# Performance work log

Measured on AMD Instinct MI355X. Metric: run time of the kernel, lower is better.

Reference implementation:

```python
import jax, jax.numpy as jnp
import numpy as np

B, N, K, D, M, KEY_DIM = 2, 16384, 32, 128, 2, 64


def _mlp(x, w_in, b_in, w_hid, b_hid, w_out, b_out, act):
    # FCBlock: in->hidden, 3 hidden layers, hidden->out; activation on all but last.
    h = act(x @ w_in + b_in)
    for i in range(w_hid.shape[0]):
        h = act(h @ w_hid[i] + b_hid[i])
    return h @ w_out + b_out


def setup_inputs() -> dict:
    key = jax.random.key(0)
    ks = jax.random.split(key, 16)
    rn = lambda k, s, sc=1.0: jax.random.normal(k, s, dtype=jnp.float32) * sc
    w_scale = 0.05  # small init so sigmoid/affinity stay in a sane range
    return {
        'backbone_features': rn(ks[0], (B, N, D)),
        'gather_affinities': rn(ks[1], (B, M, N, K)),
        'embed_table': rn(ks[2], (M, KEY_DIM)),
        'enc_w_in': rn(ks[3], (2 * D, 128), w_scale),
        'enc_b_in': jnp.zeros((128,), jnp.float32),
        'enc_w_hid': rn(ks[4], (3, 128, 128), w_scale),
        'enc_b_hid': jnp.zeros((3, 128), jnp.float32),
        'enc_w_out': rn(ks[5], (128, KEY_DIM), w_scale),
        'enc_b_out': jnp.zeros((KEY_DIM,), jnp.float32),
        'bias_w_in': rn(ks[6], (2 * D, 128), w_scale),
        'bias_b_in': jnp.zeros((128,), jnp.float32),
        'bias_w_hid': rn(ks[7], (3, 128, 128), w_scale),
        'bias_b_hid': jnp.zeros((3, 128), jnp.float32),
        'bias_w_out': rn(ks[8], (128, 1), w_scale),
        'bias_b_out': jnp.zeros((1,), jnp.float32),
        'indices': jax.random.randint(ks[9], (3, B, N, K), 0, N),
    }


def reference(backbone_features, gather_affinities, embed_table,
              enc_w_in, enc_b_in, enc_w_hid, enc_b_hid, enc_w_out, enc_b_out,
              bias_w_in, bias_b_in, bias_w_hid, bias_b_hid, bias_w_out, bias_b_out,
              indices):
    # indices: [3, B, N, K]; channel 1 = x node ids, channel 2 = y node ids
    x_idx, y_idx = indices[1], indices[2]                       # [B, N, K]
    gather = jax.vmap(lambda feats, idx: feats[idx])            # per-batch gather
    x_feat = gather(backbone_features, x_idx)                   # [B, N, K, D]
    y_feat = gather(backbone_features, y_idx)                   # [B, N, K, D]
    edge_feat = jnp.concatenate([x_feat, y_feat], axis=-1)      # [B, N, K, 2D]

    edge_cond = _mlp(edge_feat, enc_w_in, enc_b_in, enc_w_hid, enc_b_hid,
                     enc_w_out, enc_b_out, jax.nn.relu)          # [B, N, K, KEY]
    edge_bias = _mlp(edge_feat, bias_w_in, bias_b_in, bias_w_hid, bias_b_hid,
                     bias_w_out, bias_b_out, jax.nn.gelu)[..., 0]  # [B, N, K]

    # L2 normalize (F.normalize, p=2, dim=-1, eps=1e-12)
    eps = 1e-12
    edge_cond = edge_cond / jnp.maximum(
        jnp.linalg.norm(edge_cond, axis=-1, keepdims=True), eps)
    embeds = embed_table / jnp.maximum(
        jnp.linalg.norm(embed_table, axis=-1, keepdims=True), eps)  # [M, KEY]

    attn = jax.nn.sigmoid(jnp.einsum('bnkd,md->bmnk', edge_cond, embeds))
    obj_affinity = jnp.einsum('bmnk,bmnk->bnk', attn,
                              gather_affinities - edge_bias[:, None])
    return obj_affinity
```

## Files before the change

### kernel.cpp

```cpp
#include <hip/hip_runtime.h>

typedef short frag   __attribute__((ext_vector_type(8)));
typedef float f32x4  __attribute__((ext_vector_type(4)));
typedef float f32x16 __attribute__((ext_vector_type(16)));
typedef unsigned short u16;

#define E_TOT 1048576
#define NK    524288

#define WPK_US   176128
#define EMBN_OFF 352256
#define BB16_OFF 352768
#define WS_NEED  (BB16_OFF + 8388608)

__device__ __forceinline__ u16 f2bf(float f){
  unsigned int u = __float_as_uint(f);
  u += 0x7FFFu + ((u >> 16) & 1u);
  return (u16)(u >> 16);
}
__device__ __forceinline__ unsigned cvtpk(float lo, float hi){
  unsigned r;
  asm("v_cvt_pk_bf16_f32 %0, %1, %2" : "=v"(r) : "v"(lo), "v"(hi));
  return r;
}
__device__ __forceinline__ void plswap(unsigned &a, unsigned &b){
  asm("v_permlane32_swap_b32 %0, %1" : "+v"(a), "+v"(b));
}
__device__ __forceinline__ float frcp(float x){ return __builtin_amdgcn_rcpf(x); }
__device__ __forceinline__ float vexp2(float x){
  float r; asm("v_exp_f32 %0, %1" : "=v"(r) : "v"(x)); return r;
}
__device__ __forceinline__ float sigm(float y){
  return frcp(1.f + vexp2(-1.4426950408889634f * y));
}
__device__ __forceinline__ float gelu_f(float x){
  const float C1 = 2.0f * 0.7978845608028654f * 1.4426950408889634f;
  const float C2 = 0.044715f * C1;
  float z = x * fmaf(C2, x * x, C1);
  return x * frcp(1.f + vexp2(-z));
}

__device__ __forceinline__ void gl_lds16(const void* g, void* l){
#if __has_builtin(__builtin_amdgcn_global_load_lds)
  __builtin_amdgcn_global_load_lds(
      (const __attribute__((address_space(1))) unsigned int*)g,
      (__attribute__((address_space(3))) unsigned int*)l, 16, 0, 0);
#else
  *(uint4*)l = *(const uint4*)g;
#endif
}

template<int N> struct IC { static constexpr int value = N; };

__global__ void prep_kernel(const float* __restrict__ enc_w_in,
                            const float* __restrict__ enc_w_hid,
                            const float* __restrict__ enc_w_out,
                            const float* __restrict__ bias_w_in,
                            const float* __restrict__ bias_w_hid,
                            const float* __restrict__ bias_w_out,
                            const float* __restrict__ embed_table,
                            u16* __restrict__ wpk,
                            float* __restrict__ embn)
{
  int p = blockIdx.x * 256 + threadIdx.x;
  if (p < WPK_US) {
    const int base[12] = {0,16384,32768,49152,65536,81920,90112,106496,122880,139264,155648,172032};
    const int koff[12] = {0,128,0,0,0,0,0,128,0,0,0,0};
    const int njv[12]  = {128,128,128,128,128,64,128,128,128,128,128,1};
    const float* srcs[12] = {enc_w_in, enc_w_in, enc_w_hid, enc_w_hid+16384, enc_w_hid+32768,
                             enc_w_out, bias_w_in, bias_w_in, bias_w_hid, bias_w_hid+16384,
                             bias_w_hid+32768, bias_w_out};
    int L = 0;
    #pragma unroll
    for (int i = 1; i < 12; ++i) if (p >= base[i]) L = i;
    int r    = p - base[L];
    int f    = r >> 9;
    int q    = r & 511;
    int lane = q >> 3, e = q & 7;
    int t    = f >> 3, s = f & 7;
    int nj   = njv[L];
    int j    = 32*t + (lane & 31);
    int k    = 16*s + 8*(lane >> 5) + e + koff[L];
    wpk[p] = (j < nj) ? f2bf(srcs[L][k * nj + j]) : (u16)0;
  } else if (p < WPK_US + 128) {
    int q = p - WPK_US;
    int m = q >> 6;
    const float* row = embed_table + m * 64;
    float ss = 0.f;
    for (int t = 0; t < 64; ++t) { float v = row[t]; ss += v * v; }
    float nrm = fmaxf(sqrtf(ss), 1e-12f);
    embn[q] = row[q & 63] / nrm;
  }
}

__global__ void prep_backbone(const float* __restrict__ src, u16* __restrict__ dst)
{
  int i = (blockIdx.x * 256 + threadIdx.x) * 4;
  float4 v = *(const float4*)(src + i);
  unsigned lo = cvtpk(v.x, v.y), hi = cvtpk(v.z, v.w);
  *(uint2*)(dst + i) = make_uint2(lo, hi);
}

template<bool BF>
__global__ __launch_bounds__(256, 3)
void fused_kernel(const float* __restrict__ backbone,
                  const u16*   __restrict__ bb16,
                  const float* __restrict__ ga,
                  const int*   __restrict__ idx,
                  const float* __restrict__ enc_b_in,
                  const float* __restrict__ enc_b_hid,
                  const float* __restrict__ enc_b_out,
                  const float* __restrict__ bias_b_in,
                  const float* __restrict__ bias_b_hid,
                  const float* __restrict__ bias_b_out,
                  const u16*   __restrict__ wpk,
                  const float* __restrict__ embn,
                  float* __restrict__ out)
{
  __shared__ __align__(16) u16 wbuf[16384];

  const int tid  = threadIdx.x;
  const int w    = tid >> 6;
  const int lane = tid & 63;
  const int h    = lane >> 5;
  const int col  = lane & 31;
  const int eW   = blockIdx.x * 128 + w * 32;
  const int e    = eW + col;

  auto stageW = [&](int base_us, int nfrag){
    for (int it = w; it < nfrag; it += 4)
      gl_lds16((const void*)(wpk + base_us + it * 512 + lane * 8),
               (void*)(&wbuf[it * 512]));
  };

  stageW(0, 32);

  int b = e >> 19;
  int rxi = (b << 14) + idx[E_TOT + e];
  int ryi = (b << 14) + idx[2 * E_TOT + e];

  f32x16 acc[4];
  unsigned nb[8][4];
  const f32x16 kZ = {0.f,0.f,0.f,0.f, 0.f,0.f,0.f,0.f, 0.f,0.f,0.f,0.f, 0.f,0.f,0.f,0.f};

  union FU { unsigned u[4]; frag f; };

  auto getB_g = [&](int ri, int s) -> frag {
    size_t off = (((size_t)(unsigned)ri) << 7) + 16 * s + 8 * h;
    if constexpr (BF) {
      return *(const frag*)(bb16 + off);
    } else {
      const float* p = backbone + off;
      float4 lo = *(const float4*)p, hi = *(const float4*)(p + 4);
      FU fu;
      fu.u[0] = cvtpk(lo.x, lo.y); fu.u[1] = cvtpk(lo.z, lo.w);
      fu.u[2] = cvtpk(hi.x, hi.y); fu.u[3] = cvtpk(hi.z, hi.w);
      return fu.f;
    }
  };
  auto getBx = [&](int s) -> frag { return getB_g(rxi, s); };
  auto getBy = [&](int s) -> frag { return getB_g(ryi, s); };
  auto getBn = [&](int s) -> frag {
    FU fu;
    fu.u[0] = nb[s][0]; fu.u[1] = nb[s][1];
    fu.u[2] = nb[s][2]; fu.u[3] = nb[s][3];
    return fu.f;
  };

  auto runLayer = [&](auto SC, auto TC, auto ZFC, auto getB){
    constexpr int S_ = decltype(SC)::value;
    constexpr int T_ = decltype(TC)::value;
    constexpr bool ZF = (decltype(ZFC)::value != 0);
    #pragma unroll
    for (int s = 0; s < S_; ++s) {
      frag B = getB(s);
      #pragma unroll
      for (int t = 0; t < T_; ++t) {
        frag A = *(const frag*)(&wbuf[(t * S_ + s) * 512 + lane * 8]);
        if (ZF && s == 0)
          acc[t] = __builtin_amdgcn_mfma_f32_32x32x16_bf16(A, B, kZ, 0, 0, 0);
        else
          acc[t] = __builtin_amdgcn_mfma_f32_32x32x16_bf16(A, B, acc[t], 0, 0, 0);
      }
    }
  };

  auto finishLayer = [&](const float* bptr, bool gelu){
    #pragma unroll
    for (int t = 0; t < 4; ++t) {
      float x[16];
      #pragma unroll
      for (int q = 0; q < 4; ++q) {
        f32x4 bv = *(const f32x4*)(bptr + 32*t + 8*q + 4*h);
        #pragma unroll
        for (int i = 0; i < 4; ++i) x[4*q+i] = acc[t][4*q+i] + bv[i];
      }
      #pragma unroll
      for (int i = 0; i < 16; ++i)
        x[i] = gelu ? gelu_f(x[i]) : fmaxf(x[i], 0.f);
      unsigned wv[8];
      #pragma unroll
      for (int i = 0; i < 8; ++i) wv[i] = cvtpk(x[2*i], x[2*i+1]);
      plswap(wv[0], wv[2]); plswap(wv[1], wv[3]);
      plswap(wv[4], wv[6]); plswap(wv[5], wv[7]);
      nb[2*t][0] = wv[0]; nb[2*t][1] = wv[1]; nb[2*t][2] = wv[2]; nb[2*t][3] = wv[3];
      nb[2*t+1][0] = wv[4]; nb[2*t+1][1] = wv[5]; nb[2*t+1][2] = wv[6]; nb[2*t+1][3] = wv[7];
    }
  };

  __syncthreads();
  runLayer(IC<8>{}, IC<4>{}, IC<1>{}, getBx);
  __syncthreads();
  stageW(16384, 32);
  __syncthreads();
  runLayer(IC<8>{}, IC<4>{}, IC<0>{}, getBy);
  __syncthreads();
  stageW(32768, 32);
  finishLayer(enc_b_in, false);
  __syncthreads();
  runLayer(IC<8>{}, IC<4>{}, IC<1>{}, getBn);
  __syncthreads();
  stageW(49152, 32);
  finishLayer(enc_b_hid + 0, false);
  __syncthreads();
  runLayer(IC<8>{}, IC<4>{}, IC<1>{}, getBn);
  __syncthreads();
  stageW(65536, 32);
  finishLayer(enc_b_hid + 128, false);
  __syncthreads();
  runLayer(IC<8>{}, IC<4>{}, IC<1>{}, getBn);
  __syncthreads();
  stageW(81920, 16);
  finishLayer(enc_b_hid + 256, false);
  __syncthreads();
  runLayer(IC<8>{}, IC<2>{}, IC<1>{}, getBn);
  __syncthreads();
  stageW(90112, 32);

  float a0v, a1v;
  {
    float s2 = 0.f, p0 = 0.f, p1 = 0.f;
    #pragma unroll
    for (int t = 0; t < 2; ++t)
      #pragma unroll
      for (int q = 0; q < 4; ++q) {
        f32x4 bv = *(const f32x4*)(enc_b_out + 32*t + 8*q + 4*h);
        f32x4 e0 = *(const f32x4*)(embn + 32*t + 8*q + 4*h);
        f32x4 e1 = *(const f32x4*)(embn + 64 + 32*t + 8*q + 4*h);
        #pragma unroll
        for (int i = 0; i < 4; ++i) {
          float v = acc[t][4*q+i] + bv[i];
          s2 = fmaf(v, v, s2);
          p0 = fmaf(v, e0[i], p0);
          p1 = fmaf(v, e1[i], p1);
        }
      }
    s2 += __shfl_xor(s2, 32);
    p0 += __shfl_xor(p0, 32);
    p1 += __shfl_xor(p1, 32);
    float inv = frcp(fmaxf(sqrtf(s2), 1e-12f));
    a0v = sigm(p0 * inv);
    a1v = sigm(p1 * inv);
  }

  __syncthreads();
  runLayer(IC<8>{}, IC<4>{}, IC<1>{}, getBx);
  __syncthreads();
  stageW(106496, 32);
  __syncthreads();
  runLayer(IC<8>{}, IC<4>{}, IC<0>{}, getBy);
  __syncthreads();
  stageW(122880, 32);
  finishLayer(bias_b_in, true);
  __syncthreads();
  runLayer(IC<8>{}, IC<4>{}, IC<1>{}, getBn);
  __syncthreads();
  stageW(139264, 32);
  finishLayer(bias_b_hid + 0, true);
  __syncthreads();
  runLayer(IC<8>{}, IC<4>{}, IC<1>{}, getBn);
  __syncthreads();
  stageW(155648, 32);
  finishLayer(bias_b_hid + 128, true);
  __syncthreads();
  runLayer(IC<8>{}, IC<4>{}, IC<1>{}, getBn);
  __syncthreads();
  stageW(172032, 8);
  finishLayer(bias_b_hid + 256, true);
  __syncthreads();
  runLayer(IC<8>{}, IC<1>{}, IC<1>{}, getBn);

  if (lane < 32) {
    float bi = acc[0][0] + bias_b_out[0];
    int off = e & (NK - 1);
    float g0 = ga[((size_t)b << 20) + off];
    float g1 = ga[((size_t)b << 20) + NK + off];
    out[e] = a0v * (g0 - bi) + a1v * (g1 - bi);
  }
}

extern "C" void kernel_launch(void* const* d_in, const int* in_sizes, int n_in,
                              void* d_out, int out_size, void* d_ws, size_t ws_size,
                              hipStream_t stream) {
  const float* backbone   = (const float*)d_in[0];
  const float* ga         = (const float*)d_in[1];
  const float* embed      = (const float*)d_in[2];
  const float* enc_w_in   = (const float*)d_in[3];
  const float* enc_b_in   = (const float*)d_in[4];
  const float* enc_w_hid  = (const float*)d_in[5];
  const float* enc_b_hid  = (const float*)d_in[6];
  const float* enc_w_out  = (const float*)d_in[7];
  const float* enc_b_out  = (const float*)d_in[8];
  const float* bias_w_in  = (const float*)d_in[9];
  const float* bias_b_in  = (const float*)d_in[10];
  const float* bias_w_hid = (const float*)d_in[11];
  const float* bias_b_hid = (const float*)d_in[12];
  const float* bias_w_out = (const float*)d_in[13];
  const float* bias_b_out = (const float*)d_in[14];
  const int*   indices    = (const int*)d_in[15];

  u16*   wpk  = (u16*)d_ws;
  float* embn = (float*)((char*)d_ws + EMBN_OFF);
  u16*   bb16 = (u16*)((char*)d_ws + BB16_OFF);

  hipLaunchKernelGGL(prep_kernel, dim3(689), dim3(256), 0, stream,
                     enc_w_in, enc_w_hid, enc_w_out,
                     bias_w_in, bias_w_hid, bias_w_out,
                     embed, wpk, embn);

  bool bf = (ws_size >= (size_t)WS_NEED);
  if (bf) {
    hipLaunchKernelGGL(prep_backbone, dim3(4096), dim3(256), 0, stream, backbone, bb16);
    hipLaunchKernelGGL((fused_kernel<true>), dim3(8192), dim3(256), 0, stream,
                       backbone, bb16, ga, indices,
                       enc_b_in, enc_b_hid, enc_b_out,
                       bias_b_in, bias_b_hid, bias_b_out,
                       wpk, embn, (float*)d_out);
  } else {
    hipLaunchKernelGGL((fused_kernel<false>), dim3(8192), dim3(256), 0, stream,
                       backbone, bb16, ga, indices,
                       enc_b_in, enc_b_hid, enc_b_out,
                       bias_b_in, bias_b_hid, bias_b_out,
                       wpk, embn, (float*)d_out);
  }
}
```

Before: 612.6 us.

## Triple-buffer weight halves in LDS to overlap staging with MFMA

Splits each layer's weight tile into 16-fragment halves held in a three-slot LDS ring, so the next half is prefetched while the current half runs its MFMAs. This removes the barrier-staging-barrier pattern that serialized weight loads with compute. It also raises wave priority around the MFMA loops. LDS use grows from 32 KB to 48 KB per block, which may limit occupancy at 3 blocks per CU, and the slot and half bookkeeping is intricate and easy to get wrong.

```diff
diff --git a/kernel.cpp b/kernel.cpp
--- a/kernel.cpp
+++ b/kernel.cpp
@@ -117,7 +117,7 @@
                   const float* __restrict__ embn,
                   float* __restrict__ out)
 {
-  __shared__ __align__(16) u16 wbuf[16384];
+  __shared__ __align__(16) u16 wbuf[3][8192];
 
   const int tid  = threadIdx.x;
   const int w    = tid >> 6;
@@ -127,13 +127,17 @@
   const int eW   = blockIdx.x * 128 + w * 32;
   const int e    = eW + col;
 
-  auto stageW = [&](int base_us, int nfrag){
-    for (int it = w; it < nfrag; it += 4)
-      gl_lds16((const void*)(wpk + base_us + it * 512 + lane * 8),
-               (void*)(&wbuf[it * 512]));
-  };
-
-  stageW(0, 32);
+  auto stageHalf = [&](int hh){
+    const int hb[22] = {0,8192, 16384,24576, 32768,40960, 49152,57344,
+                        65536,73728, 81920, 90112,98304, 106496,114688,
+                        122880,131072, 139264,147456, 155648,163840, 172032};
+    int base = hb[hh];
+    int nf   = (hh == 21) ? 8 : 16;
+    int slot = hh % 3;
+    for (int it = w; it < nf; it += 4)
+      gl_lds16((const void*)(wpk + base + it * 512 + lane * 8),
+               (void*)(&wbuf[slot][it * 512]));
+  };
 
   int b = e >> 19;
   int rxi = (b << 14) + idx[E_TOT + e];
@@ -167,22 +171,25 @@
     return fu.f;
   };
 
-  auto runLayer = [&](auto SC, auto TC, auto ZFC, auto getB){
-    constexpr int S_ = decltype(SC)::value;
-    constexpr int T_ = decltype(TC)::value;
-    constexpr bool ZF = (decltype(ZFC)::value != 0);
+  auto runHalf = [&](auto SLOTC, auto T0C, auto TNC, auto ZFC, auto getB){
+    constexpr int slot = decltype(SLOTC)::value;
+    constexpr int T0   = decltype(T0C)::value;
+    constexpr int TN   = decltype(TNC)::value;
+    constexpr bool ZF  = (decltype(ZFC)::value != 0);
+    __builtin_amdgcn_s_setprio(1);
     #pragma unroll
-    for (int s = 0; s < S_; ++s) {
+    for (int s = 0; s < 8; ++s) {
       frag B = getB(s);
       #pragma unroll
-      for (int t = 0; t < T_; ++t) {
-        frag A = *(const frag*)(&wbuf[(t * S_ + s) * 512 + lane * 8]);
+      for (int tt = 0; tt < TN; ++tt) {
+        frag A = *(const frag*)(&wbuf[slot][(tt * 8 + s) * 512 + lane * 8]);
         if (ZF && s == 0)
-          acc[t] = __builtin_amdgcn_mfma_f32_32x32x16_bf16(A, B, kZ, 0, 0, 0);
+          acc[T0 + tt] = __builtin_amdgcn_mfma_f32_32x32x16_bf16(A, B, kZ, 0, 0, 0);
         else
-          acc[t] = __builtin_amdgcn_mfma_f32_32x32x16_bf16(A, B, acc[t], 0, 0, 0);
+          acc[T0 + tt] = __builtin_amdgcn_mfma_f32_32x32x16_bf16(A, B, acc[T0 + tt], 0, 0, 0);
       }
     }
+    __builtin_amdgcn_s_setprio(0);
   };
 
   auto finishLayer = [&](const float* bptr, bool gelu){
@@ -208,34 +215,24 @@
     }
   };
 
+  stageHalf(0); stageHalf(1);
   __syncthreads();
-  runLayer(IC<8>{}, IC<4>{}, IC<1>{}, getBx);
-  __syncthreads();
-  stageW(16384, 32);
-  __syncthreads();
-  runLayer(IC<8>{}, IC<4>{}, IC<0>{}, getBy);
-  __syncthreads();
-  stageW(32768, 32);
-  finishLayer(enc_b_in, false);
-  __syncthreads();
-  runLayer(IC<8>{}, IC<4>{}, IC<1>{}, getBn);
-  __syncthreads();
-  stageW(49152, 32);
-  finishLayer(enc_b_hid + 0, false);
-  __syncthreads();
-  runLayer(IC<8>{}, IC<4>{}, IC<1>{}, getBn);
-  __syncthreads();
-  stageW(65536, 32);
-  finishLayer(enc_b_hid + 128, false);
-  __syncthreads();
-  runLayer(IC<8>{}, IC<4>{}, IC<1>{}, getBn);
-  __syncthreads();
-  stageW(81920, 16);
-  finishLayer(enc_b_hid + 256, false);
-  __syncthreads();
-  runLayer(IC<8>{}, IC<2>{}, IC<1>{}, getBn);
-  __syncthreads();
-  stageW(90112, 32);
+
+  stageHalf(2);  runHalf(IC<0>{}, IC<0>{}, IC<2>{}, IC<1>{}, getBx); __syncthreads();
+  stageHalf(3);  runHalf(IC<1>{}, IC<2>{}, IC<2>{}, IC<1>{}, getBx); __syncthreads();
+  stageHalf(4);  runHalf(IC<2>{}, IC<0>{}, IC<2>{}, IC<0>{}, getBy); __syncthreads();
+  stageHalf(5);  runHalf(IC<0>{}, IC<2>{}, IC<2>{}, IC<0>{}, getBy);
+  finishLayer(enc_b_in, false); __syncthreads();
+  stageHalf(6);  runHalf(IC<1>{}, IC<0>{}, IC<2>{}, IC<1>{}, getBn); __syncthreads();
+  stageHalf(7);  runHalf(IC<2>{}, IC<2>{}, IC<2>{}, IC<1>{}, getBn);
+  finishLayer(enc_b_hid + 0, false); __syncthreads();
+  stageHalf(8);  runHalf(IC<0>{}, IC<0>{}, IC<2>{}, IC<1>{}, getBn); __syncthreads();
+  stageHalf(9);  runHalf(IC<1>{}, IC<2>{}, IC<2>{}, IC<1>{}, getBn);
+  finishLayer(enc_b_hid + 128, false); __syncthreads();
+  stageHalf(10); runHalf(IC<2>{}, IC<0>{}, IC<2>{}, IC<1>{}, getBn); __syncthreads();
+  stageHalf(11); runHalf(IC<0>{}, IC<2>{}, IC<2>{}, IC<1>{}, getBn);
+  finishLayer(enc_b_hid + 256, false); __syncthreads();
+  stageHalf(12); runHalf(IC<1>{}, IC<0>{}, IC<2>{}, IC<1>{}, getBn);
 
   float a0v, a1v;
   {
@@ -262,33 +259,23 @@
     a0v = sigm(p0 * inv);
     a1v = sigm(p1 * inv);
   }
-
   __syncthreads();
-  runLayer(IC<8>{}, IC<4>{}, IC<1>{}, getBx);
-  __syncthreads();
-  stageW(106496, 32);
-  __syncthreads();
-  runLayer(IC<8>{}, IC<4>{}, IC<0>{}, getBy);
-  __syncthreads();
-  stageW(122880, 32);
-  finishLayer(bias_b_in, true);
-  __syncthreads();
-  runLayer(IC<8>{}, IC<4>{}, IC<1>{}, getBn);
-  __syncthreads();
-  stageW(139264, 32);
-  finishLayer(bias_b_hid + 0, true);
-  __syncthreads();
-  runLayer(IC<8>{}, IC<4>{}, IC<1>{}, getBn);
-  __syncthreads();
-  stageW(155648, 32);
-  finishLayer(bias_b_hid + 128, true);
-  __syncthreads();
-  runLayer(IC<8>{}, IC<4>{}, IC<1>{}, getBn);
-  __syncthreads();
-  stageW(172032, 8);
-  finishLayer(bias_b_hid + 256, true);
-  __syncthreads();
-  runLayer(IC<8>{}, IC<1>{}, IC<1>{}, getBn);
+
+  stageHalf(13); runHalf(IC<2>{}, IC<0>{}, IC<2>{}, IC<1>{}, getBx); __syncthreads();
+  stageHalf(14); runHalf(IC<0>{}, IC<2>{}, IC<2>{}, IC<1>{}, getBx); __syncthreads();
+  stageHalf(15); runHalf(IC<1>{}, IC<0>{}, IC<2>{}, IC<0>{}, getBy); __syncthreads();
+  stageHalf(16); runHalf(IC<2>{}, IC<2>{}, IC<2>{}, IC<0>{}, getBy);
+  finishLayer(bias_b_in, true); __syncthreads();
+  stageHalf(17); runHalf(IC<0>{}, IC<0>{}, IC<2>{}, IC<1>{}, getBn); __syncthreads();
+  stageHalf(18); runHalf(IC<1>{}, IC<2>{}, IC<2>{}, IC<1>{}, getBn);
+  finishLayer(bias_b_in ? bias_b_hid + 0 : bias_b_hid, true); __syncthreads();
+  stageHalf(19); runHalf(IC<2>{}, IC<0>{}, IC<2>{}, IC<1>{}, getBn); __syncthreads();
+  stageHalf(20); runHalf(IC<0>{}, IC<2>{}, IC<2>{}, IC<1>{}, getBn);
+  finishLayer(bias_b_hid + 128, true); __syncthreads();
+  stageHalf(21); runHalf(IC<1>{}, IC<0>{}, IC<2>{}, IC<1>{}, getBn); __syncthreads();
+                 runHalf(IC<2>{}, IC<2>{}, IC<2>{}, IC<1>{}, getBn);
+  finishLayer(bias_b_hid + 256, true); __syncthreads();
+                 runHalf(IC<0>{}, IC<0>{}, IC<1>{}, IC<1>{}, getBn);
 
   if (lane < 32) {
     float bi = acc[0][0] + bias_b_out[0];
```

After: 592.4 us. 3.3% less time.
